# Kernel tuning notes

Hardware: AMD Instinct MI355X
Metric: run time of the kernel (lower is better)

Reference implementation:

```python
import jax, jax.numpy as jnp
import numpy as np

# Dimensions (see shape_source)
B, NCAM, J = 2, 6, 23          # batch, cameras, joints
HM = 160                        # heatmap crop side (half-res)
W, H = 640, 512                 # padded canvas (img_size[0], img_size[1])
D = 50                          # 3D grid side = grid_size/grid_spacing/2
GRID_SIZE = 200.0               # cfg.VORTEX.ROI_CUBE_SIZE
GRID_SPACING = 2.0              # cfg.VORTEX.GRID_SPACING


def setup_inputs() -> dict:
    key = jax.random.key(0)
    k1, k2, k3, k4, k5 = jax.random.split(key, 5)
    heatmaps_batch = jax.random.normal(k1, (B, NCAM, J, HM, HM), jnp.float32)
    # centers in full-res pixel coords such that the crop fits inside the canvas
    cx = jax.random.randint(k2, (B, NCAM, 1), HM, 2 * W - HM)
    cy = jax.random.randint(k3, (B, NCAM, 1), HM, 2 * H - HM)
    centerHM = jnp.concatenate([cx, cy], axis=-1).astype(jnp.int32)
    heatmap_vol = jax.random.normal(k4, (B, J, D, D, D), jnp.float32)  # v2vNet output
    center3D = jax.random.normal(k5, (B, 1, 3), jnp.float32) * 10.0
    return {
        "heatmaps_batch": heatmaps_batch,
        "heatmap_vol": heatmap_vol,
        "center3D": center3D,
        "centerHM": centerHM,
    }


def reference(heatmaps_batch, heatmap_vol, center3D, centerHM):
    # --- dynamic per-sample heatmap placement (replaces the F.pad loops) ---
    def place(hm, c):  # hm: [J, HM, HM], c: [2] int32
        x0 = c[0] // 2 - HM // 2
        y0 = c[1] // 2 - HM // 2
        canvas = jnp.zeros((J, H, W), hm.dtype)
        return jax.lax.dynamic_update_slice(canvas, hm, (jnp.int32(0), y0, x0))

    heatmaps_padded = jax.vmap(jax.vmap(place))(heatmaps_batch, centerHM)  # [B,NCAM,J,H,W]

    # --- 3D soft-argmax over the volumetric heatmap ---
    heatmap_final = jax.nn.softplus(heatmap_vol)            # [B, J, D, D, D]
    norm = heatmap_final.sum(axis=(2, 3, 4))                # [B, J]
    idx = jnp.arange(D, dtype=heatmap_final.dtype)
    # marginalize then dot with index grid (same math as mul with meshgrid + sum)
    mx = heatmap_final.sum(axis=(3, 4))                     # varies along grid dim 0 (xx)
    my = heatmap_final.sum(axis=(2, 4))                     # grid dim 1 (yy)
    mz = heatmap_final.sum(axis=(2, 3))                     # grid dim 2 (zz)
    x = (mx * idx).sum(-1) / norm
    y = (my * idx).sum(-1) / norm
    z = (mz * idx).sum(-1) / norm
    points3D = jnp.stack([x, y, z], axis=2)                 # [B, J, 3]
    points3D = points3D * GRID_SPACING * 2.0 - GRID_SIZE / GRID_SPACING + center3D
    return (heatmap_final, heatmaps_padded, points3D)
```

## Files before the change

kernel.cpp:

```cpp
#include <hip/hip_runtime.h>

#define B_    2
#define NCAM_ 6
#define J_    23
#define HM_   160
#define W_    640
#define H_    512
#define D_    50

static constexpr long long HF_SIZE = (long long)B_ * J_ * D_ * D_ * D_;
static constexpr long long HP_SIZE = (long long)B_ * NCAM_ * J_ * H_ * W_;
static constexpr int NBJ = B_ * J_;
static constexpr int CHUNKS = 32;
static constexpr int SP_BLOCKS = NBJ * CHUNKS;
static constexpr int NPLANES = B_ * NCAM_ * J_;
static constexpr int W4 = W_ / 4;
static constexpr int PLANE_F4 = H_ * W4;
static constexpr int INT_F4 = HM_ * W4;
static constexpr int EXT_F4 = PLANE_F4 - INT_F4;
static constexpr int EXTB_PER_PLANE = 16;
static constexpr int INTB_PER_PLANE = 8;
static constexpr int EXT_BLOCKS = NPLANES * EXTB_PER_PLANE;
static constexpr int INT_BLOCKS = NPLANES * INTB_PER_PLANE;
static constexpr int TOTAL_BLOCKS = SP_BLOCKS + EXT_BLOCKS + INT_BLOCKS;

__global__ void fused_all(const float4* __restrict__ vol4,
                          float4* __restrict__ out_hf4,
                          float* __restrict__ partials,
                          const float* __restrict__ hm,
                          const int* __restrict__ centerHM,
                          float4* __restrict__ out_pad4) {
    const int gid = blockIdx.x;

    if (gid < SP_BLOCKS) {
        const int NE4 = (D_ * D_ * D_) / 4;
        const int bj = gid / CHUNKS;
        const int chunk = gid % CHUNKS;
        const long long base4 = (long long)bj * NE4;

        float s = 0.f, sx = 0.f, sy = 0.f, sz = 0.f;
        for (int i = chunk * blockDim.x + threadIdx.x; i < NE4; i += CHUNKS * blockDim.x) {
            const float4 v = vol4[base4 + i];
            float4 sp;
            sp.x = fmaxf(v.x, 0.f) + log1pf(__expf(-fabsf(v.x)));
            sp.y = fmaxf(v.y, 0.f) + log1pf(__expf(-fabsf(v.y)));
            sp.z = fmaxf(v.z, 0.f) + log1pf(__expf(-fabsf(v.z)));
            sp.w = fmaxf(v.w, 0.f) + log1pf(__expf(-fabsf(v.w)));
            out_hf4[base4 + i] = sp;
            const int e0 = i * 4;
            const int t0 = e0 / D_;       const int z0 = e0 - t0 * D_;
            const int x0i = t0 / D_;      const int y0i = t0 - x0i * D_;
            const int e2 = e0 + 2;
            const int t2 = e2 / D_;       const int z2 = e2 - t2 * D_;
            const int x2i = t2 / D_;      const int y2i = t2 - x2i * D_;
            const float p01 = sp.x + sp.y;
            const float p23 = sp.z + sp.w;
            s  += p01 + p23;
            sx += p01 * (float)x0i + p23 * (float)x2i;
            sy += p01 * (float)y0i + p23 * (float)y2i;
            sz += sp.x * (float)z0 + sp.y * (float)(z0 + 1)
                + sp.z * (float)z2 + sp.w * (float)(z2 + 1);
        }

        #pragma unroll
        for (int off = 32; off > 0; off >>= 1) {
            s  += __shfl_down(s,  off, 64);
            sx += __shfl_down(sx, off, 64);
            sy += __shfl_down(sy, off, 64);
            sz += __shfl_down(sz, off, 64);
        }
        __shared__ float sm[4][4];
        const int lane = threadIdx.x & 63;
        const int wid  = threadIdx.x >> 6;
        if (lane == 0) {
            sm[0][wid] = s; sm[1][wid] = sx; sm[2][wid] = sy; sm[3][wid] = sz;
        }
        __syncthreads();
        if (threadIdx.x == 0) {
            float a0 = 0.f, a1 = 0.f, a2 = 0.f, a3 = 0.f;
            #pragma unroll
            for (int w = 0; w < 4; ++w) {
                a0 += sm[0][w]; a1 += sm[1][w]; a2 += sm[2][w]; a3 += sm[3][w];
            }
            partials[gid * 4 + 0] = a0;
            partials[gid * 4 + 1] = a1;
            partials[gid * 4 + 2] = a2;
            partials[gid * 4 + 3] = a3;
        }
        return;
    }

    if (gid < SP_BLOCKS + EXT_BLOCKS) {
        const int pb    = gid - SP_BLOCKS;
        const int plane = pb >> 4;
        const int sub   = pb & (EXTB_PER_PLANE - 1);
        const int bcam  = plane / J_;

        const int cy = centerHM[bcam * 2 + 1];
        int y0 = cy / 2 - HM_ / 2;
        y0 = min(max(y0, 0), H_ - HM_);
        const int top = y0 * W4;

        float4* __restrict__ outp = out_pad4 + (long long)plane * PLANE_F4;
        const float4 z = make_float4(0.f, 0.f, 0.f, 0.f);
        const int e_end = min((sub + 1) * (EXT_F4 / EXTB_PER_PLANE), EXT_F4);
        for (int e = sub * (EXT_F4 / EXTB_PER_PLANE) + threadIdx.x; e < e_end; e += 256) {
            const int dst = e < top ? e : e + INT_F4;
            outp[dst] = z;
        }
        return;
    }

    {
        const int pb    = gid - SP_BLOCKS - EXT_BLOCKS;
        const int plane = pb >> 3;
        const int sub   = pb & (INTB_PER_PLANE - 1);
        const int bcam  = plane / J_;

        const int cx = centerHM[bcam * 2 + 0];
        const int cy = centerHM[bcam * 2 + 1];
        int x0 = cx / 2 - HM_ / 2;
        int y0 = cy / 2 - HM_ / 2;
        x0 = min(max(x0, 0), W_ - HM_);
        y0 = min(max(y0, 0), H_ - HM_);

        const float* __restrict__ src = hm + (long long)plane * (HM_ * HM_);
        float4* __restrict__ outp = out_pad4 + (long long)plane * PLANE_F4 + y0 * W4;

        const int i_end = min((sub + 1) * (INT_F4 / INTB_PER_PLANE), INT_F4);
        for (int i = sub * (INT_F4 / INTB_PER_PLANE) + threadIdx.x; i < i_end; i += 256) {
            const int dy = i / W4;
            const int f  = i - dy * W4;
            const int dxb = (f << 2) - x0;
            const float* __restrict__ row = src + dy * HM_;
            float4 v;
            #pragma unroll
            for (int k = 0; k < 4; ++k) {
                const int dx = dxb + k;
                const int dxc = min(max(dx, 0), HM_ - 1);
                const float val = row[dxc];
                (&v.x)[k] = ((unsigned)dx < (unsigned)HM_) ? val : 0.f;
            }
            outp[i] = v;
        }
    }
}

__global__ void finalize_points(const float* __restrict__ partials,
                                const float* __restrict__ c3d,
                                float* __restrict__ out_p3d) {
    const int bj = threadIdx.x;
    if (bj < NBJ) {
        const int b = bj / J_;
        float a0 = 0.f, a1 = 0.f, a2 = 0.f, a3 = 0.f;
        for (int c = 0; c < CHUNKS; ++c) {
            const float* p = &partials[(bj * CHUNKS + c) * 4];
            a0 += p[0]; a1 += p[1]; a2 += p[2]; a3 += p[3];
        }
        const float inv = 1.0f / a0;
        out_p3d[bj * 3 + 0] = a1 * inv * 4.0f - 100.0f + c3d[b * 3 + 0];
        out_p3d[bj * 3 + 1] = a2 * inv * 4.0f - 100.0f + c3d[b * 3 + 1];
        out_p3d[bj * 3 + 2] = a3 * inv * 4.0f - 100.0f + c3d[b * 3 + 2];
    }
}

extern "C" void kernel_launch(void* const* d_in, const int* in_sizes, int n_in,
                              void* d_out, int out_size, void* d_ws, size_t ws_size,
                              hipStream_t stream) {
    const float* hm_batch  = (const float*)d_in[0];
    const float* vol       = (const float*)d_in[1];
    const float* c3d       = (const float*)d_in[2];
    const int*   centerHM  = (const int*)d_in[3];

    float* out     = (float*)d_out;
    float* out_hf  = out;
    float* out_pad = out + HF_SIZE;
    float* out_p3d = out + HF_SIZE + HP_SIZE;

    float* partials = (float*)d_ws;

    fused_all<<<TOTAL_BLOCKS, 256, 0, stream>>>(
        (const float4*)vol, (float4*)out_hf, partials,
        hm_batch, centerHM, (float4*)out_pad);

    finalize_points<<<1, 64, 0, stream>>>(partials, c3d, out_p3d);
}
```

Measured before the change: 102.7 us.

## Copy heatmap rows per wavefront with float4 loads and lane shuffles for misalignment

Rewrites the interior-band placement so each wavefront handles whole rows. It loads the 160-wide source row as 40 float4 values and realigns them to the destination's sub-float4 offset with __shfl_up, replacing per-element scalar gathers with clamped indexing. The interior blocks are also moved to the front of the grid so they are dispatched before the softplus and exterior-zero blocks. The cost is more per-row scalar overhead and idle lanes, since only 40 of 64 lanes load and 41 store.

```diff
diff --git a/kernel.cpp b/kernel.cpp
--- a/kernel.cpp
+++ b/kernel.cpp
@@ -15,27 +15,80 @@
 static constexpr int SP_BLOCKS = NBJ * CHUNKS;
 static constexpr int NPLANES = B_ * NCAM_ * J_;
 static constexpr int W4 = W_ / 4;
+static constexpr int HM4 = HM_ / 4;
 static constexpr int PLANE_F4 = H_ * W4;
 static constexpr int INT_F4 = HM_ * W4;
 static constexpr int EXT_F4 = PLANE_F4 - INT_F4;
 static constexpr int EXTB_PER_PLANE = 16;
-static constexpr int INTB_PER_PLANE = 8;
 static constexpr int EXT_BLOCKS = NPLANES * EXTB_PER_PLANE;
-static constexpr int INT_BLOCKS = NPLANES * INTB_PER_PLANE;
-static constexpr int TOTAL_BLOCKS = SP_BLOCKS + EXT_BLOCKS + INT_BLOCKS;
+static constexpr int INT_ROWS = NPLANES * HM_;
+static constexpr int ROWS_PER_WAVE = 16;
+static constexpr int INT_BLOCKS = INT_ROWS / (4 * ROWS_PER_WAVE);
+static constexpr int TOTAL_BLOCKS = INT_BLOCKS + SP_BLOCKS + EXT_BLOCKS;
 
 __global__ void fused_all(const float4* __restrict__ vol4,
                           float4* __restrict__ out_hf4,
                           float* __restrict__ partials,
-                          const float* __restrict__ hm,
+                          const float4* __restrict__ hm4,
                           const int* __restrict__ centerHM,
                           float4* __restrict__ out_pad4) {
     const int gid = blockIdx.x;
 
-    if (gid < SP_BLOCKS) {
+    if (gid < INT_BLOCKS) {
+        const int wgl  = gid * 4 + (threadIdx.x >> 6);
+        const int lane = threadIdx.x & 63;
+        const float4 z = make_float4(0.f, 0.f, 0.f, 0.f);
+
+        for (int rr = 0; rr < ROWS_PER_WAVE; ++rr) {
+            const int row   = wgl * ROWS_PER_WAVE + rr;
+            const int plane = row / HM_;
+            const int dy    = row - plane * HM_;
+            const int bcam  = plane / J_;
+
+            const int cx = centerHM[bcam * 2 + 0];
+            const int cy = centerHM[bcam * 2 + 1];
+            int x0 = min(max(cx / 2 - HM_ / 2, 0), W_ - HM_);
+            int y0 = min(max(cy / 2 - HM_ / 2, 0), H_ - HM_);
+            const int q = x0 >> 2;
+            const int r = x0 & 3;
+            const int nspan = r ? (HM4 + 1) : HM4;
+
+            const float4* __restrict__ src4 =
+                hm4 + (long long)plane * (HM_ * HM4) + dy * HM4;
+            float4* __restrict__ outrow =
+                out_pad4 + (long long)plane * PLANE_F4 + (y0 + dy) * W4;
+
+            float4 s = z;
+            if (lane < HM4) s = src4[lane];
+            float px = __shfl_up(s.x, 1, 64);
+            float py = __shfl_up(s.y, 1, 64);
+            float pz = __shfl_up(s.z, 1, 64);
+            float pw = __shfl_up(s.w, 1, 64);
+            if (lane == 0) { px = py = pz = pw = 0.f; }
+
+            float4 v;
+            switch (r) {
+                case 0:  v = s; break;
+                case 1:  v = make_float4(pw, s.x, s.y, s.z); break;
+                case 2:  v = make_float4(pz, pw, s.x, s.y); break;
+                default: v = make_float4(py, pz, pw, s.x); break;
+            }
+            if (lane < nspan) outrow[q + lane] = v;
+
+            const int cnt = W4 - nspan;
+            const int z0i = lane;
+            if (z0i < cnt) outrow[z0i < q ? z0i : z0i + nspan] = z;
+            const int z1i = lane + 64;
+            if (z1i < cnt) outrow[z1i < q ? z1i : z1i + nspan] = z;
+        }
+        return;
+    }
+
+    if (gid < INT_BLOCKS + SP_BLOCKS) {
+        const int sg = gid - INT_BLOCKS;
         const int NE4 = (D_ * D_ * D_) / 4;
-        const int bj = gid / CHUNKS;
-        const int chunk = gid % CHUNKS;
+        const int bj = sg / CHUNKS;
+        const int chunk = sg % CHUNKS;
         const long long base4 = (long long)bj * NE4;
 
         float s = 0.f, sx = 0.f, sy = 0.f, sz = 0.f;
@@ -82,66 +135,30 @@
             for (int w = 0; w < 4; ++w) {
                 a0 += sm[0][w]; a1 += sm[1][w]; a2 += sm[2][w]; a3 += sm[3][w];
             }
-            partials[gid * 4 + 0] = a0;
-            partials[gid * 4 + 1] = a1;
-            partials[gid * 4 + 2] = a2;
-            partials[gid * 4 + 3] = a3;
+            partials[sg * 4 + 0] = a0;
+            partials[sg * 4 + 1] = a1;
+            partials[sg * 4 + 2] = a2;
+            partials[sg * 4 + 3] = a3;
         }
         return;
     }
 
-    if (gid < SP_BLOCKS + EXT_BLOCKS) {
-        const int pb    = gid - SP_BLOCKS;
+    {
+        const int pb    = gid - INT_BLOCKS - SP_BLOCKS;
         const int plane = pb >> 4;
         const int sub   = pb & (EXTB_PER_PLANE - 1);
         const int bcam  = plane / J_;
 
         const int cy = centerHM[bcam * 2 + 1];
-        int y0 = cy / 2 - HM_ / 2;
-        y0 = min(max(y0, 0), H_ - HM_);
+        int y0 = min(max(cy / 2 - HM_ / 2, 0), H_ - HM_);
         const int top = y0 * W4;
 
         float4* __restrict__ outp = out_pad4 + (long long)plane * PLANE_F4;
         const float4 z = make_float4(0.f, 0.f, 0.f, 0.f);
-        const int e_end = min((sub + 1) * (EXT_F4 / EXTB_PER_PLANE), EXT_F4);
+        const int e_end = (sub + 1) * (EXT_F4 / EXTB_PER_PLANE);
         for (int e = sub * (EXT_F4 / EXTB_PER_PLANE) + threadIdx.x; e < e_end; e += 256) {
             const int dst = e < top ? e : e + INT_F4;
             outp[dst] = z;
-        }
-        return;
-    }
-
-    {
-        const int pb    = gid - SP_BLOCKS - EXT_BLOCKS;
-        const int plane = pb >> 3;
-        const int sub   = pb & (INTB_PER_PLANE - 1);
-        const int bcam  = plane / J_;
-
-        const int cx = centerHM[bcam * 2 + 0];
-        const int cy = centerHM[bcam * 2 + 1];
-        int x0 = cx / 2 - HM_ / 2;
-        int y0 = cy / 2 - HM_ / 2;
-        x0 = min(max(x0, 0), W_ - HM_);
-        y0 = min(max(y0, 0), H_ - HM_);
-
-        const float* __restrict__ src = hm + (long long)plane * (HM_ * HM_);
-        float4* __restrict__ outp = out_pad4 + (long long)plane * PLANE_F4 + y0 * W4;
-
-        const int i_end = min((sub + 1) * (INT_F4 / INTB_PER_PLANE), INT_F4);
-        for (int i = sub * (INT_F4 / INTB_PER_PLANE) + threadIdx.x; i < i_end; i += 256) {
-            const int dy = i / W4;
-            const int f  = i - dy * W4;
-            const int dxb = (f << 2) - x0;
-            const float* __restrict__ row = src + dy * HM_;
-            float4 v;
-            #pragma unroll
-            for (int k = 0; k < 4; ++k) {
-                const int dx = dxb + k;
-                const int dxc = min(max(dx, 0), HM_ - 1);
-                const float val = row[dxc];
-                (&v.x)[k] = ((unsigned)dx < (unsigned)HM_) ? val : 0.f;
-            }
-            outp[i] = v;
         }
     }
 }
@@ -181,7 +198,7 @@
 
     fused_all<<<TOTAL_BLOCKS, 256, 0, stream>>>(
         (const float4*)vol, (float4*)out_hf, partials,
-        hm_batch, centerHM, (float4*)out_pad);
+        (const float4*)hm_batch, centerHM, (float4*)out_pad);
 
     finalize_points<<<1, 64, 0, stream>>>(partials, c3d, out_p3d);
 }
```

Result: faster. 96.71 us (-5.9%).
